# Kernel optimization log

Hardware: AMD Instinct MI355X
Metric: run time of the kernel (lower is better)

The kernel has to match this reference:

```python
import jax, jax.numpy as jnp
import numpy as np
from jax import lax

B, E, H, L, P, IMG, NCLS = 8, 768, 12, 12, 16, 224, 1000
D = E // H
MLP = 4 * E
SCALE = D ** -0.5
NPATCH = (IMG // P) ** 2  # 196
N = NPATCH + 1             # 197 with cls token
INIT_VAL = 0.1


def _ln(x, g, b, eps=1e-5):
    mu = jnp.mean(x, -1, keepdims=True)
    var = jnp.mean((x - mu) ** 2, -1, keepdims=True)
    return (x - mu) / jnp.sqrt(var + eps) * g + b


def _wasserstein(q, cov_q, k, cov_k):
    # 2-Wasserstein distance matrix between diagonal Gaussians (STOSA style)
    mean_term = (-2.0 * jnp.einsum('bhnd,bhmd->bhnm', q, k)
                 + jnp.sum(q * q, -1)[..., :, None]
                 + jnp.sum(k * k, -1)[..., None, :])
    sq_q = jnp.sqrt(jnp.clip(cov_q, 1e-24))
    sq_k = jnp.sqrt(jnp.clip(cov_k, 1e-24))
    cov_term = (-2.0 * jnp.einsum('bhnd,bhmd->bhnm', sq_q, sq_k)
                + jnp.sum(cov_q, -1)[..., :, None]
                + jnp.sum(cov_k, -1)[..., None, :])
    return mean_term + cov_term


def _patch_embed(x, w, b):
    # x: [B,3,IMG,IMG], w: [E,3,P,P] -> [B, NPATCH, E]
    y = lax.conv_general_dilated(x, w, (P, P), 'VALID',
                                 dimension_numbers=('NCHW', 'OIHW', 'NCHW'))
    y = y + b[None, :, None, None]
    return y.reshape(x.shape[0], E, -1).transpose(0, 2, 1)


def _mlp(x, w1, b1, w2, b2):
    return jax.nn.gelu(x @ w1.T + b1, approximate=False) @ w2.T + b2


def setup_inputs() -> dict:
    key = jax.random.key(0)
    ks = jax.random.split(key, 32)
    s = 0.02
    inp = {
        'x': jax.random.normal(ks[0], (B, 3, IMG, IMG), jnp.float32),
        'rel_pos_bias': jax.random.normal(ks[1], (H, N, N), jnp.float32),
        'patch_w': jax.random.normal(ks[2], (E, 3, P, P), jnp.float32) * s,
        'patch_b': jnp.zeros((E,), jnp.float32),
        'cov_patch_w': jax.random.normal(ks[3], (E, 3, P, P), jnp.float32) * s,
        'cov_patch_b': jnp.zeros((E,), jnp.float32),
        'cls_tok': jax.random.normal(ks[4], (1, 1, E), jnp.float32) * s,
        'cov_cls_tok': jax.random.normal(ks[5], (1, 1, E), jnp.float32) * s,
        'norm1_g': jnp.ones((L, E), jnp.float32),
        'norm1_b': jnp.zeros((L, E), jnp.float32),
        'qkv_w': jax.random.normal(ks[6], (L, 3 * E, E), jnp.float32) * s,
        'q_bias': jnp.zeros((L, E), jnp.float32),
        'v_bias': jnp.zeros((L, E), jnp.float32),
        'cov_q_bias': jnp.zeros((L, E), jnp.float32),
        'cov_v_bias': jnp.zeros((L, E), jnp.float32),
        'proj_w': jax.random.normal(ks[7], (L, E, E), jnp.float32) * s,
        'proj_b': jnp.zeros((L, E), jnp.float32),
        'cov_proj_w': jax.random.normal(ks[8], (L, E, E), jnp.float32) * s,
        'cov_proj_b': jnp.zeros((L, E), jnp.float32),
        'gamma1': jnp.full((L, E), INIT_VAL, jnp.float32),
        'gamma2': jnp.full((L, E), INIT_VAL, jnp.float32),
        'norm2_g': jnp.ones((L, E), jnp.float32),
        'norm2_b': jnp.zeros((L, E), jnp.float32),
        'fc1_w': jax.random.normal(ks[9], (L, MLP, E), jnp.float32) * s,
        'fc1_b': jnp.zeros((L, MLP), jnp.float32),
        'fc2_w': jax.random.normal(ks[10], (L, E, MLP), jnp.float32) * s,
        'fc2_b': jnp.zeros((L, E), jnp.float32),
        'fc_norm_g': jnp.ones((E,), jnp.float32),
        'fc_norm_b': jnp.zeros((E,), jnp.float32),
        'head_w': jax.random.normal(ks[11], (NCLS, E), jnp.float32) * s,
        'head_b': jnp.zeros((NCLS,), jnp.float32),
    }
    # fix_init_weight rescaling: proj / cov_proj / fc2 divided by sqrt(2*layer_id)
    resc = 1.0 / jnp.sqrt(2.0 * jnp.arange(1, L + 1, dtype=jnp.float32))
    inp['proj_w'] = inp['proj_w'] * resc[:, None, None]
    inp['cov_proj_w'] = inp['cov_proj_w'] * resc[:, None, None]
    inp['fc2_w'] = inp['fc2_w'] * resc[:, None, None]
    return inp


def reference(x, rel_pos_bias, patch_w, patch_b, cov_patch_w, cov_patch_b,
              cls_tok, cov_cls_tok, norm1_g, norm1_b, qkv_w, q_bias, v_bias,
              cov_q_bias, cov_v_bias, proj_w, proj_b, cov_proj_w, cov_proj_b,
              gamma1, gamma2, norm2_g, norm2_b, fc1_w, fc1_b, fc2_w, fc2_b,
              fc_norm_g, fc_norm_b, head_w, head_b):
    b = x.shape[0]
    xm = _patch_embed(x, patch_w, patch_b)
    xc = _patch_embed(x, cov_patch_w, cov_patch_b)
    xm = jnp.concatenate([jnp.broadcast_to(cls_tok, (b, 1, E)), xm], 1)
    xc = jnp.concatenate([jnp.broadcast_to(cov_cls_tok, (b, 1, E)), xc], 1)
    n = xm.shape[1]

    for i in range(L):
        xm_n = _ln(xm, norm1_g[i], norm1_b[i])
        xc_n = _ln(xc, norm1_g[i], norm1_b[i])  # shared norm1, as in source
        qkvb = jnp.concatenate([q_bias[i], jnp.zeros_like(v_bias[i]), v_bias[i]])
        cov_qkvb = jnp.concatenate([cov_q_bias[i], jnp.zeros_like(cov_v_bias[i]), cov_v_bias[i]])
        qkv = (xm_n @ qkv_w[i].T + qkvb).reshape(b, n, 3, H, D).transpose(2, 0, 3, 1, 4)
        q, k, v = qkv[0], qkv[1], qkv[2]
        # NOTE: source (bug-faithfully) uses qkv.weight for the cov path too
        cqkv = jax.nn.elu(xc_n @ qkv_w[i].T + cov_qkvb) + 1.0
        cqkv = cqkv.reshape(b, n, 3, H, D).transpose(2, 0, 3, 1, 4)
        cq, ck, cv = cqkv[0], cqkv[1], cqkv[2]
        q = q * SCALE
        attn = jax.nn.sigmoid(-_wasserstein(q, cq, k, ck) + 1e-24)
        attn = jax.nn.softmax(attn + rel_pos_bias, axis=-1)  # [B,H,N,N]
        mean_ctx = jnp.einsum('bhnm,bhmd->bhnd', attn, v).transpose(0, 2, 1, 3).reshape(b, n, E)
        cov_ctx = jnp.einsum('bhnm,bhmd->bhnd', attn * attn, cv).transpose(0, 2, 1, 3).reshape(b, n, E)
        mh = mean_ctx @ proj_w[i].T + proj_b[i]
        ch = cov_ctx @ cov_proj_w[i].T + cov_proj_b[i]
        xm = xm + gamma1[i] * mh
        xm = xm + gamma2[i] * _mlp(_ln(xm, norm2_g[i], norm2_b[i]), fc1_w[i], fc1_b[i], fc2_w[i], fc2_b[i])
        xc = xc + gamma1[i] * ch
        xc = xc + gamma2[i] * _mlp(_ln(xc, norm2_g[i], norm2_b[i]), fc1_w[i], fc1_b[i], fc2_w[i], fc2_b[i])

    t = jnp.mean(xm[:, 1:], axis=1)          # mean pooling over patch tokens
    t = _ln(t, fc_norm_g, fc_norm_b)
    return t @ head_w.T + head_b              # [B, num_classes]
```

## Files before the change

### kernel.cpp

```cpp
#include <hip/hip_runtime.h>
#include <hip/hip_bf16.h>
#include <math.h>

#define BB 8
#define EE 768
#define HH 12
#define LL 12
#define DD 64
#define MLPD 3072
#define NN 197
#define NPATCH 196
#define NCLS 1000
#define NROWS (BB*NN)
#define PROWS (BB*NPATCH)
#define MPAD 1664
#define HTILES 13
#define NBH (BB*HH)
#define NP224 224
#define NP256 256
#define SCALE 0.125f

#define MODE_F32   0
#define MODE_ELU1F 1
#define MODE_GELUB 2
#define MODE_RESF  3

typedef __attribute__((ext_vector_type(8))) short bf16x8;
typedef __attribute__((ext_vector_type(4))) float f32x4;

__device__ __forceinline__ unsigned short f2b(float f) {
    union { __hip_bfloat16 h; unsigned short u; } x;
    x.h = __float2bfloat16(f);
    return x.u;
}

__device__ __forceinline__ float b2f(unsigned short u) {
    union { unsigned int i; float f; } x;
    x.i = ((unsigned int)u) << 16;
    return x.f;
}

#define GLD(gptr, lptr) __builtin_amdgcn_global_load_lds( \
    (const __attribute__((address_space(1))) unsigned int*)(gptr), \
    (__attribute__((address_space(3))) unsigned int*)(lptr), 16, 0, 0)

__global__ __launch_bounds__(256) void mfma_gemm2(
    const unsigned short* __restrict__ A0, const unsigned short* __restrict__ A1,
    const unsigned short* __restrict__ W0, const unsigned short* __restrict__ W1,
    const float* __restrict__ bias0, const float* __restrict__ bias1,
    int K, int Nc, int mode0, int mode1,
    const float* __restrict__ gamma,
    const float* __restrict__ resid0, const float* __restrict__ resid1,
    float* __restrict__ Cf0, float* __restrict__ Cf1,
    unsigned short* __restrict__ Cb0, unsigned short* __restrict__ Cb1)
{
    __shared__ unsigned short lA[2][128 * 32];
    __shared__ unsigned short lB[2][128 * 32];
    const int tid  = threadIdx.x;
    const int lane = tid & 63;
    const int wave = tid >> 6;
    const int wm = wave >> 1, wn = wave & 1;
    const int half = blockIdx.y >= HTILES;
    const int mout0 = (blockIdx.y - (half ? HTILES : 0)) * 128;
    const int n0 = blockIdx.x * 128;
    const unsigned short* A = half ? A1 : A0;
    const unsigned short* W = half ? W1 : W0;
    const float* bias = half ? bias1 : bias0;
    const float* resid = half ? resid1 : resid0;
    float* Cf = half ? Cf1 : Cf0;
    unsigned short* Cb = half ? Cb1 : Cb0;
    const int mode = half ? mode1 : mode0;

    const int srow  = lane >> 2;
    const int skoff = (lane & 3) * 8;
    const int fr = lane & 15;
    const int fk = (lane >> 4) * 8;

    auto stage = [&](int bufi, int k0) {
#pragma unroll
        for (int i = 0; i < 2; i++) {
            int chunk = wave * 2 + i;
            int row = chunk * 16 + srow;
            GLD(A + (size_t)(mout0 + row) * K + k0 + skoff, &lA[bufi][chunk * 512]);
            GLD(W + (size_t)(n0 + row) * K + k0 + skoff, &lB[bufi][chunk * 512]);
        }
    };

    f32x4 acc[4][4];
#pragma unroll
    for (int i = 0; i < 4; i++)
#pragma unroll
        for (int j = 0; j < 4; j++) acc[i][j] = (f32x4){0.f, 0.f, 0.f, 0.f};

    const int NT = K >> 5;
    stage(0, 0);
    __syncthreads();
    int cur = 0;
    for (int t = 0; t < NT; t++) {
        if (t + 1 < NT) stage(cur ^ 1, (t + 1) * 32);
        bf16x8 a[4], b[4];
#pragma unroll
        for (int q = 0; q < 4; q++) {
            a[q] = *(const bf16x8*)(&lA[cur][(wm * 64 + q * 16 + fr) * 32 + fk]);
            b[q] = *(const bf16x8*)(&lB[cur][(wn * 64 + q * 16 + fr) * 32 + fk]);
        }
#pragma unroll
        for (int i = 0; i < 4; i++)
#pragma unroll
            for (int j = 0; j < 4; j++)
                acc[i][j] = __builtin_amdgcn_mfma_f32_16x16x32_bf16(a[i], b[j], acc[i][j], 0, 0, 0);
        __syncthreads();
        cur ^= 1;
    }

    const int crow0 = mout0 + wm * 64;
    const int ccol0 = n0 + wn * 64;
    const int lr = (lane >> 4) * 4;
    const int lc = lane & 15;
#pragma unroll
    for (int i = 0; i < 4; i++) {
#pragma unroll
        for (int j = 0; j < 4; j++) {
            int col = ccol0 + j * 16 + lc;
            float bv = bias ? bias[col] : 0.f;
#pragma unroll
            for (int r = 0; r < 4; r++) {
                int row = crow0 + i * 16 + lr + r;
                float v = acc[i][j][r] + bv;
                size_t o = (size_t)row * Nc + col;
                if (mode == MODE_ELU1F) {
                    Cf[o] = (v > 0.f) ? (v + 1.f) : expf(v);
                } else if (mode == MODE_GELUB) {
                    v = 0.5f * v * (1.f + erff(v * 0.70710678118654752f));
                    Cb[o] = f2b(v);
                } else if (mode == MODE_RESF) {
                    Cf[o] = resid[o] + gamma[col] * v;
                } else {
                    Cf[o] = v;
                }
            }
        }
    }
}

__global__ __launch_bounds__(256) void mfma_gemm2_sk(
    const unsigned short* __restrict__ A0, const unsigned short* __restrict__ A1,
    const unsigned short* __restrict__ W0, const unsigned short* __restrict__ W1,
    int K, int Kc, int Nc, int S,
    float* __restrict__ P)
{
    __shared__ unsigned short lA[2][128 * 32];
    __shared__ unsigned short lB[2][128 * 32];
    const int tid  = threadIdx.x;
    const int lane = tid & 63;
    const int wave = tid >> 6;
    const int wm = wave >> 1, wn = wave & 1;
    const int half = blockIdx.y >= HTILES;
    const int mout0 = (blockIdx.y - (half ? HTILES : 0)) * 128;
    const int n0 = blockIdx.x * 128;
    const int z = blockIdx.z;
    const int kb = z * Kc;
    const unsigned short* A = half ? A1 : A0;
    const unsigned short* W = half ? W1 : W0;

    const int srow  = lane >> 2;
    const int skoff = (lane & 3) * 8;
    const int fr = lane & 15;
    const int fk = (lane >> 4) * 8;

    auto stage = [&](int bufi, int k0) {
#pragma unroll
        for (int i = 0; i < 2; i++) {
            int chunk = wave * 2 + i;
            int row = chunk * 16 + srow;
            GLD(A + (size_t)(mout0 + row) * K + k0 + skoff, &lA[bufi][chunk * 512]);
            GLD(W + (size_t)(n0 + row) * K + k0 + skoff, &lB[bufi][chunk * 512]);
        }
    };

    f32x4 acc[4][4];
#pragma unroll
    for (int i = 0; i < 4; i++)
#pragma unroll
        for (int j = 0; j < 4; j++) acc[i][j] = (f32x4){0.f, 0.f, 0.f, 0.f};

    const int NT = Kc >> 5;
    stage(0, kb);
    __syncthreads();
    int cur = 0;
    for (int t = 0; t < NT; t++) {
        if (t + 1 < NT) stage(cur ^ 1, kb + (t + 1) * 32);
        bf16x8 a[4], b[4];
#pragma unroll
        for (int q = 0; q < 4; q++) {
            a[q] = *(const bf16x8*)(&lA[cur][(wm * 64 + q * 16 + fr) * 32 + fk]);
            b[q] = *(const bf16x8*)(&lB[cur][(wn * 64 + q * 16 + fr) * 32 + fk]);
        }
#pragma unroll
        for (int i = 0; i < 4; i++)
#pragma unroll
            for (int j = 0; j < 4; j++)
                acc[i][j] = __builtin_amdgcn_mfma_f32_16x16x32_bf16(a[i], b[j], acc[i][j], 0, 0, 0);
        __syncthreads();
        cur ^= 1;
    }

    float* Pout = P + (size_t)(half * S + z) * MPAD * Nc;
    const int crow0 = mout0 + wm * 64;
    const int ccol0 = n0 + wn * 64;
    const int lr = (lane >> 4) * 4;
    const int lc = lane & 15;
#pragma unroll
    for (int i = 0; i < 4; i++) {
#pragma unroll
        for (int j = 0; j < 4; j++) {
            int col = ccol0 + j * 16 + lc;
#pragma unroll
            for (int r = 0; r < 4; r++) {
                int row = crow0 + i * 16 + lr + r;
                Pout[(size_t)row * Nc + col] = acc[i][j][r];
            }
        }
    }
}

__global__ __launch_bounds__(256) void sk_reduce_kernel(
    const float* __restrict__ P, int S, int Nc,
    const float* __restrict__ bias0, const float* __restrict__ bias1,
    float* __restrict__ C0, float* __restrict__ C1)
{
    const size_t per = (size_t)MPAD * Nc;
    size_t gi = ((size_t)blockIdx.x * 256 + threadIdx.x) * 4;
    if (gi >= per) return;
    const int half = blockIdx.y;
    const float* p = P + (size_t)half * S * per + gi;
    float4 s = *(const float4*)p;
    for (int z = 1; z < S; z++) {
        float4 q = *(const float4*)(p + (size_t)z * per);
        s.x += q.x; s.y += q.y; s.z += q.z; s.w += q.w;
    }
    const int col = (int)(gi % (size_t)Nc);
    const float* bias = half ? bias1 : bias0;
    float4 bv = *(const float4*)(bias + col);
    s.x += bv.x; s.y += bv.y; s.z += bv.z; s.w += bv.w;
    float* C = half ? C1 : C0;
    *(float4*)(C + gi) = s;
}

__global__ __launch_bounds__(256) void sk_reduce_ln(
    const float* __restrict__ P, int S,
    const float* __restrict__ bias0, const float* __restrict__ bias1,
    const float* __restrict__ gamma,
    const float* __restrict__ resid0, const float* __restrict__ resid1,
    float* __restrict__ C0, float* __restrict__ C1,
    const float* __restrict__ lnG, const float* __restrict__ lnB,
    unsigned short* __restrict__ Y)
{
    const int row = blockIdx.x;
    const int half = blockIdx.y;
    const int tid = threadIdx.x;
    const size_t per = (size_t)MPAD * EE;
    const float* p = P + (size_t)half * S * per + (size_t)row * EE;
    const float* bias = half ? bias1 : bias0;
    const float* resid = half ? resid1 : resid0;
    float* C = half ? C1 : C0;
    float v[3];
#pragma unroll
    for (int i = 0; i < 3; i++) {
        int e = tid + i * 256;
        float s = p[e];
        for (int z = 1; z < S; z++) s += p[(size_t)z * per + e];
        v[i] = resid[(size_t)row * EE + e] + gamma[e] * (s + bias[e]);
        C[(size_t)row * EE + e] = v[i];
    }
    if (!Y) return;
    __shared__ float red[256];
    red[tid] = v[0] + v[1] + v[2];
    __syncthreads();
    for (int s2 = 128; s2 > 0; s2 >>= 1) { if (tid < s2) red[tid] += red[tid + s2]; __syncthreads(); }
    float mu = red[0] * (1.f / 768.f);
    __syncthreads();
    float d0 = v[0] - mu, d1 = v[1] - mu, d2 = v[2] - mu;
    red[tid] = d0 * d0 + d1 * d1 + d2 * d2;
    __syncthreads();
    for (int s2 = 128; s2 > 0; s2 >>= 1) { if (tid < s2) red[tid] += red[tid + s2]; __syncthreads(); }
    float rstd = rsqrtf(red[0] * (1.f / 768.f) + 1e-5f);
    unsigned short* yr = Y + ((size_t)half * MPAD + row) * EE;
    yr[tid]       = f2b(d0 * rstd * lnG[tid]       + lnB[tid]);
    yr[tid + 256] = f2b(d1 * rstd * lnG[tid + 256] + lnB[tid + 256]);
    yr[tid + 512] = f2b(d2 * rstd * lnG[tid + 512] + lnB[tid + 512]);
}

__global__ __launch_bounds__(256) void pre_kernel(
    const float* __restrict__ qkv, const float* __restrict__ cqkv,
    unsigned short* __restrict__ Aq, unsigned short* __restrict__ Bk,
    float* __restrict__ rsum, float* __restrict__ csum,
    unsigned short* __restrict__ vT, unsigned short* __restrict__ cvT)
{
    const int t = blockIdx.x;
    const int bh = blockIdx.y;
    const int b = bh / HH, h = bh % HH;
    const int n0 = t * 64;
    const int lane = threadIdx.x & 63;
    const int w = threadIdx.x >> 6;
    __shared__ unsigned short vs[64][66];
    __shared__ unsigned short cvs[64][66];

    for (int p = 0; p < 16; p++) {
        int nl = p * 4 + w;
        int n = n0 + nl;
        int d = lane;
        size_t arow = ((size_t)bh * NP256 + n) * 128;
        if (n < NN) {
            size_t basei = (size_t)(b * NN + n) * 3 * EE + h * DD + d;
            float q  = qkv[basei];
            float k  = qkv[basei + EE];
            float v  = qkv[basei + 2 * EE];
            float cq = cqkv[basei];
            float ck = cqkv[basei + EE];
            float cv = cqkv[basei + 2 * EE];
            float qs = q * SCALE;
            float sqq = sqrtf(fmaxf(cq, 1e-24f));
            float sqk = sqrtf(fmaxf(ck, 1e-24f));
            Aq[arow + d]      = f2b(qs);
            Aq[arow + 64 + d] = f2b(sqq);
            Bk[arow + d]      = f2b(k);
            Bk[arow + 64 + d] = f2b(sqk);
            vs[nl][d]  = f2b(v);
            cvs[nl][d] = f2b(cv);
            float r = qs * qs + cq;
            float c = k * k + ck;
            for (int off2 = 32; off2 > 0; off2 >>= 1) {
                r += __shfl_down(r, off2);
                c += __shfl_down(c, off2);
            }
            if (d == 0) { rsum[bh * NP256 + n] = r; csum[bh * NP256 + n] = c; }
        } else {
            ((unsigned int*)(Aq + arow))[d] = 0u;
            ((unsigned int*)(Bk + arow))[d] = 0u;
            vs[nl][d] = 0; cvs[nl][d] = 0;
            if (d == 0) { rsum[bh * NP256 + n] = 0.f; csum[bh * NP256 + n] = 0.f; }
        }
    }
    __syncthreads();
    for (int p = 0; p < 16; p++) {
        int dr = p * 4 + w;
        int n = n0 + lane;
        if (n < NP224) {
            vT [((size_t)bh * 64 + dr) * NP224 + n] = vs[lane][dr];
            cvT[((size_t)bh * 64 + dr) * NP224 + n] = cvs[lane][dr];
        }
    }
}

#define PADW 232
__global__ __launch_bounds__(256) void attn_fused(
    const unsigned short* __restrict__ Aq, const unsigned short* __restrict__ Bk,
    const float* __restrict__ rsum, const float* __restrict__ csum,
    const float* __restrict__ rpb,
    const unsigned short* __restrict__ vT, const unsigned short* __restrict__ cvT,
    unsigned short* __restrict__ ctxm, unsigned short* __restrict__ ctxc)
{
    __shared__ unsigned short lA[64 * 32];
    __shared__ unsigned short lB[256 * 32];
    __shared__ unsigned short lB2[128 * 32];
    __shared__ unsigned short pL[64 * PADW];
    const int tid = threadIdx.x, lane = tid & 63, w = tid >> 6;
    const int bh = blockIdx.y;
    const int b = bh / HH, h = bh % HH;
    const int q0 = blockIdx.x * 64;
    const int srow = lane >> 2, skoff = (lane & 3) * 8;
    const int fr = lane & 15, fk = (lane >> 4) * 8;
    const int lr4 = (lane >> 4) * 4;
    const unsigned short* A = Aq + (size_t)bh * NP256 * 128;
    const unsigned short* B = Bk + (size_t)bh * NP256 * 128;

    f32x4 accS[16];
#pragma unroll
    for (int j = 0; j < 16; j++) accS[j] = (f32x4){0.f, 0.f, 0.f, 0.f};

    for (int k0 = 0; k0 < 128; k0 += 32) {
        GLD(A + (size_t)(q0 + w * 16 + srow) * 128 + k0 + skoff, lA + w * 512);
#pragma unroll
        for (int i = 0; i < 4; i++) {
            int chunk = w * 4 + i;
            GLD(B + (size_t)(chunk * 16 + srow) * 128 + k0 + skoff, lB + chunk * 512);
        }
        __syncthreads();
        bf16x8 a = *(const bf16x8*)(lA + (w * 16 + fr) * 32 + fk);
#pragma unroll
        for (int j = 0; j < 16; j++) {
            bf16x8 bb = *(const bf16x8*)(lB + (j * 16 + fr) * 32 + fk);
            accS[j] = __builtin_amdgcn_mfma_f32_16x16x32_bf16(a, bb, accS[j], 0, 0, 0);
        }
        __syncthreads();
    }

    float rs[4];
#pragma unroll
    for (int r = 0; r < 4; r++) rs[r] = rsum[bh * NP256 + q0 + w * 16 + lr4 + r];
    float cs[16];
#pragma unroll
    for (int j = 0; j < 16; j++) cs[j] = csum[bh * NP256 + j * 16 + fr];

#pragma unroll
    for (int r = 0; r < 4; r++) {
        int rowg = q0 + w * 16 + lr4 + r;
        float v[16];
#pragma unroll
        for (int j = 0; j < 16; j++) {
            int col = j * 16 + fr;
            float z = 2.f * accS[j][r] - rs[r] - cs[j] + 1e-24f;
            float s = 1.f / (1.f + expf(-z));
            float rp = (col < NN && rowg < NN) ? rpb[((size_t)h * NN + rowg) * NN + col] : 0.f;
            v[j] = (col < NN) ? (s + rp) : -1e30f;
        }
        float mx = -1e30f;
#pragma unroll
        for (int j = 0; j < 16; j++) mx = fmaxf(mx, v[j]);
        mx = fmaxf(mx, __shfl_xor(mx, 1));
        mx = fmaxf(mx, __shfl_xor(mx, 2));
        mx = fmaxf(mx, __shfl_xor(mx, 4));
        mx = fmaxf(mx, __shfl_xor(mx, 8));
        float sum = 0.f;
#pragma unroll
        for (int j = 0; j < 16; j++) { v[j] = expf(v[j] - mx); sum += v[j]; }
        sum += __shfl_xor(sum, 1);
        sum += __shfl_xor(sum, 2);
        sum += __shfl_xor(sum, 4);
        sum += __shfl_xor(sum, 8);
        float inv = 1.f / sum;
        int rowl = w * 16 + lr4 + r;
#pragma unroll
        for (int j = 0; j < 14; j++)
            pL[rowl * PADW + j * 16 + fr] = f2b(v[j] * inv);
    }

    f32x4 acc2[2][4];
#pragma unroll
    for (int p = 0; p < 2; p++)
#pragma unroll
        for (int j = 0; j < 4; j++) acc2[p][j] = (f32x4){0.f, 0.f, 0.f, 0.f};

    for (int k0 = 0; k0 < NP224; k0 += 32) {
#pragma unroll
        for (int i = 0; i < 2; i++) {
            int chunk = w * 2 + i;
            const unsigned short* src = (chunk < 4)
                ? (vT  + ((size_t)bh * 64 + chunk * 16 + srow) * NP224)
                : (cvT + ((size_t)bh * 64 + (chunk - 4) * 16 + srow) * NP224);
            GLD(src + k0 + skoff, lB2 + chunk * 512);
        }
        __syncthreads();
        bf16x8 ap = *(const bf16x8*)(pL + (w * 16 + fr) * PADW + k0 + fk);
        bf16x8 ap2;
#pragma unroll
        for (int e = 0; e < 8; e++) {
            float pv = b2f((unsigned short)ap[e]);
            ap2[e] = (short)f2b(pv * pv);
        }
#pragma unroll
        for (int j = 0; j < 4; j++) {
            bf16x8 bv = *(const bf16x8*)(lB2 + (j * 16 + fr) * 32 + fk);
            bf16x8 bc = *(const bf16x8*)(lB2 + ((64 + j * 16) + fr) * 32 + fk);
            acc2[0][j] = __builtin_amdgcn_mfma_f32_16x16x32_bf16(ap,  bv, acc2[0][j], 0, 0, 0);
            acc2[1][j] = __builtin_amdgcn_mfma_f32_16x16x32_bf16(ap2, bc, acc2[1][j], 0, 0, 0);
        }
        __syncthreads();
    }

#pragma unroll
    for (int j = 0; j < 4; j++) {
        int d = j * 16 + fr;
#pragma unroll
        for (int r = 0; r < 4; r++) {
            int n = q0 + w * 16 + lr4 + r;
            if (n >= NN) continue;
            size_t o = ((size_t)(b * NN + n)) * EE + h * DD + d;
            ctxm[o] = f2b(acc2[0][j][r]);
            ctxc[o] = f2b(acc2[1][j][r]);
        }
    }
}

__global__ __launch_bounds__(256) void head_kernel(
    const float* __restrict__ pooled, const float* __restrict__ W,
    const float* __restrict__ bias, float* __restrict__ out)
{
    const int wv = threadIdx.x >> 6, lane = threadIdx.x & 63;
    const int c = blockIdx.x * 4 + wv;
    const int b = blockIdx.y;
    if (c >= NCLS) return;
    const float* wr = W + (size_t)c * EE;
    const float* pr = pooled + (size_t)b * EE;
    float s = 0.f;
#pragma unroll
    for (int i = 0; i < 12; i++) s += pr[lane + i * 64] * wr[lane + i * 64];
    for (int off = 32; off > 0; off >>= 1) s += __shfl_down(s, off);
    if (lane == 0) out[(size_t)b * NCLS + c] = s + bias[c];
}

__global__ __launch_bounds__(256) void cvt_kernel(
    const float* __restrict__ src, unsigned short* __restrict__ dst, int n)
{
    int i = (blockIdx.x * 256 + threadIdx.x) * 4;
    if (i >= n) return;
    float4 f = *(const float4*)(src + i);
    ushort4 u;
    u.x = f2b(f.x); u.y = f2b(f.y); u.z = f2b(f.z); u.w = f2b(f.w);
    *(ushort4*)(dst + i) = u;
}

#define W_QKV   0
#define W_PROJ  1769472
#define W_CPROJ 2359296
#define W_FC1   2949120
#define W_FC2   5308416
#define W_TOTAL 7667712

__global__ __launch_bounds__(256) void cvt_all_kernel(
    const float* __restrict__ qkvw, const float* __restrict__ pw,
    const float* __restrict__ cpw, const float* __restrict__ f1,
    const float* __restrict__ f2, unsigned short* __restrict__ dst)
{
    size_t i = ((size_t)blockIdx.x * 256 + threadIdx.x) * 4;
    if (i >= (size_t)LL * W_TOTAL) return;
    int l = (int)(i / W_TOTAL);
    int r = (int)(i % W_TOTAL);
    const float* s;
    if (r < W_PROJ)        s = qkvw + (size_t)l * (3 * EE * EE) + r;
    else if (r < W_CPROJ)  s = pw   + (size_t)l * (EE * EE)     + (r - W_PROJ);
    else if (r < W_FC1)    s = cpw  + (size_t)l * (EE * EE)     + (r - W_CPROJ);
    else if (r < W_FC2)    s = f1   + (size_t)l * (MLPD * EE)   + (r - W_FC1);
    else                   s = f2   + (size_t)l * (MLPD * EE)   + (r - W_FC2);
    float4 f = *(const float4*)s;
    ushort4 u;
    u.x = f2b(f.x); u.y = f2b(f.y); u.z = f2b(f.z); u.w = f2b(f.w);
    *(ushort4*)(dst + i) = u;
}

__global__ __launch_bounds__(256) void qkvbias_all_kernel(
    const float* __restrict__ qb, const float* __restrict__ vb,
    const float* __restrict__ cqb, const float* __restrict__ cvb,
    float* __restrict__ bqc)
{
    int l = blockIdx.y;
    int j = blockIdx.x * 256 + threadIdx.x;
    if (j >= 3 * EE) return;
    float m, c;
    if (j < EE)        { m = qb[l * EE + j];          c = cqb[l * EE + j]; }
    else if (j < 2*EE) { m = 0.f;                      c = 0.f; }
    else               { m = vb[l * EE + j - 2 * EE];  c = cvb[l * EE + j - 2 * EE]; }
    bqc[(size_t)l * 4608 + j]        = m;
    bqc[(size_t)l * 4608 + 2304 + j] = c;
}

__global__ __launch_bounds__(256) void im2col_kernel(
    const float* __restrict__ x, unsigned short* __restrict__ col)
{
    int idx = blockIdx.x * 256 + threadIdx.x;
    if (idx >= PROWS * EE) return;
    int c = idx % EE;
    int r = idx / EE;
    int b = r / NPATCH;
    int p = r % NPATCH;
    int ph = p / 14, pw = p % 14;
    int ch = c >> 8;
    int rem = c & 255;
    int i = rem >> 4, j = rem & 15;
    col[idx] = f2b(x[(((size_t)b * 3 + ch) * 224 + (ph * 16 + i)) * 224 + (pw * 16 + j)]);
}

__global__ __launch_bounds__(256) void assemble_kernel(
    const float* __restrict__ tm, const float* __restrict__ tc,
    const float* __restrict__ cls, const float* __restrict__ ccls,
    float* __restrict__ xm, float* __restrict__ xc)
{
    int idx = blockIdx.x * 256 + threadIdx.x;
    if (idx >= NROWS * EE) return;
    int e = idx % EE;
    int r = idx / EE;
    int b = r / NN, n = r % NN;
    if (n == 0) {
        xm[idx] = cls[e];
        xc[idx] = ccls[e];
    } else {
        size_t s = ((size_t)(b * NPATCH + n - 1)) * EE + e;
        xm[idx] = tm[s];
        xc[idx] = tc[s];
    }
}

__global__ __launch_bounds__(256) void ln2_kernel(
    const float* __restrict__ xm, const float* __restrict__ xc,
    unsigned short* __restrict__ y, const float* __restrict__ g,
    const float* __restrict__ bb)
{
    int row = blockIdx.x;
    int tid = threadIdx.x;
    const float* src;
    size_t orow;
    if (row < NROWS) { src = xm + (size_t)row * EE; orow = row; }
    else { src = xc + (size_t)(row - NROWS) * EE; orow = (size_t)(row - NROWS) + MPAD; }
    __shared__ float red[256];
    float v0 = src[tid], v1 = src[tid + 256], v2 = src[tid + 512];
    red[tid] = v0 + v1 + v2;
    __syncthreads();
    for (int s = 128; s > 0; s >>= 1) { if (tid < s) red[tid] += red[tid + s]; __syncthreads(); }
    float mu = red[0] * (1.f / 768.f);
    __syncthreads();
    float d0 = v0 - mu, d1 = v1 - mu, d2 = v2 - mu;
    red[tid] = d0 * d0 + d1 * d1 + d2 * d2;
    __syncthreads();
    for (int s = 128; s > 0; s >>= 1) { if (tid < s) red[tid] += red[tid + s]; __syncthreads(); }
    float rstd = rsqrtf(red[0] * (1.f / 768.f) + 1e-5f);
    unsigned short* yr = y + orow * EE;
    yr[tid]       = f2b(d0 * rstd * g[tid]       + bb[tid]);
    yr[tid + 256] = f2b(d1 * rstd * g[tid + 256] + bb[tid + 256]);
    yr[tid + 512] = f2b(d2 * rstd * g[tid + 512] + bb[tid + 512]);
}

__global__ __launch_bounds__(256) void pool_ln_kernel(
    const float* __restrict__ xm, float* __restrict__ out,
    const float* __restrict__ g, const float* __restrict__ bb)
{
    int b = blockIdx.x;
    int tid = threadIdx.x;
    __shared__ float red[256];
    float p[3];
#pragma unroll
    for (int i = 0; i < 3; i++) {
        int e = tid + i * 256;
        float s = 0.f;
        for (int n = 1; n < NN; n++) s += xm[((size_t)(b * NN + n)) * EE + e];
        p[i] = s * (1.f / 196.f);
    }
    red[tid] = p[0] + p[1] + p[2];
    __syncthreads();
    for (int s = 128; s > 0; s >>= 1) { if (tid < s) red[tid] += red[tid + s]; __syncthreads(); }
    float mu = red[0] * (1.f / 768.f);
    __syncthreads();
    float d0 = p[0] - mu, d1 = p[1] - mu, d2 = p[2] - mu;
    red[tid] = d0 * d0 + d1 * d1 + d2 * d2;
    __syncthreads();
    for (int s = 128; s > 0; s >>= 1) { if (tid < s) red[tid] += red[tid + s]; __syncthreads(); }
    float rstd = rsqrtf(red[0] * (1.f / 768.f) + 1e-5f);
    out[(size_t)b * EE + tid]       = d0 * rstd * g[tid]       + bb[tid];
    out[(size_t)b * EE + tid + 256] = d1 * rstd * g[tid + 256] + bb[tid + 256];
    out[(size_t)b * EE + tid + 512] = d2 * rstd * g[tid + 512] + bb[tid + 512];
}

extern "C" void kernel_launch(void* const* d_in, const int* in_sizes, int n_in,
                              void* d_out, int out_size, void* d_ws, size_t ws_size,
                              hipStream_t stream)
{
    const float* x        = (const float*)d_in[0];
    const float* rpb      = (const float*)d_in[1];
    const float* patch_w  = (const float*)d_in[2];
    const float* patch_b  = (const float*)d_in[3];
    const float* cpatch_w = (const float*)d_in[4];
    const float* cpatch_b = (const float*)d_in[5];
    const float* cls_tok  = (const float*)d_in[6];
    const float* ccls_tok = (const float*)d_in[7];
    const float* norm1_g  = (const float*)d_in[8];
    const float* norm1_b  = (const float*)d_in[9];
    const float* qkv_w    = (const float*)d_in[10];
    const float* q_bias   = (const float*)d_in[11];
    const float* v_bias   = (const float*)d_in[12];
    const float* cq_bias  = (const float*)d_in[13];
    const float* cv_bias  = (const float*)d_in[14];
    const float* proj_w   = (const float*)d_in[15];
    const float* proj_b   = (const float*)d_in[16];
    const float* cproj_w  = (const float*)d_in[17];
    const float* cproj_b  = (const float*)d_in[18];
    const float* gamma1   = (const float*)d_in[19];
    const float* gamma2   = (const float*)d_in[20];
    const float* norm2_g  = (const float*)d_in[21];
    const float* norm2_b  = (const float*)d_in[22];
    const float* fc1_w    = (const float*)d_in[23];
    const float* fc1_b    = (const float*)d_in[24];
    const float* fc2_w    = (const float*)d_in[25];
    const float* fc2_b    = (const float*)d_in[26];
    const float* fcn_g    = (const float*)d_in[27];
    const float* fcn_b    = (const float*)d_in[28];
    const float* head_w   = (const float*)d_in[29];
    const float* head_b   = (const float*)d_in[30];
    float* out = (float*)d_out;

    char* base = (char*)d_ws;
    size_t off = 0;
    auto alloc = [&](size_t bytes) {
        void* p = base + off;
        off = (off + bytes + 255) & ~(size_t)255;
        return p;
    };
    unsigned short* wbuf  = (unsigned short*)alloc((size_t)LL * W_TOTAL * 2);
    unsigned short* pw_m  = (unsigned short*)alloc((size_t)589824 * 2);
    unsigned short* pw_c  = (unsigned short*)alloc((size_t)589824 * 2);
    float* xm   = (float*)alloc((size_t)MPAD * EE * 4);
    float* xc   = (float*)alloc((size_t)MPAD * EE * 4);
    unsigned short* xn2 = (unsigned short*)alloc((size_t)2 * MPAD * EE * 2);
    float* qkv  = (float*)alloc((size_t)MPAD * 3 * EE * 4);
    float* cqkv = (float*)alloc((size_t)MPAD * 3 * EE * 4);
    unsigned short* hbuf = (unsigned short*)alloc((size_t)2 * MPAD * MLPD * 2);
    unsigned short* Aq  = (unsigned short*)alloc((size_t)NBH * NP256 * 128 * 2);
    unsigned short* Bk  = (unsigned short*)alloc((size_t)NBH * NP256 * 128 * 2);
    unsigned short* vT  = (unsigned short*)alloc((size_t)NBH * 64 * NP224 * 2);
    unsigned short* cvT = (unsigned short*)alloc((size_t)NBH * 64 * NP224 * 2);
    float* rsum = (float*)alloc((size_t)NBH * NP256 * 4);
    float* csum = (float*)alloc((size_t)NBH * NP256 * 4);
    unsigned short* ctx2 = (unsigned short*)alloc((size_t)2 * MPAD * EE * 2);
    unsigned short* colb = (unsigned short*)alloc((size_t)MPAD * EE * 2);
    float* bqc    = (float*)alloc((size_t)LL * 2 * 2304 * 4);
    float* pooled = (float*)alloc((size_t)BB * EE * 4);
    float* pbuf = (float*)alloc((size_t)2 * 4 * MPAD * EE * 4);
    float* tm = qkv;
    float* tc = cqkv;
    unsigned short* ctxm = ctx2;
    unsigned short* ctxc = ctx2 + (size_t)MPAD * EE;

    dim3 t256(256);
    dim3 gridRedE(MPAD * EE / 1024, 2);
    dim3 gridRedLN(MPAD, 2);

    {
        size_t tot4 = (size_t)LL * W_TOTAL / 4;
        cvt_all_kernel<<<dim3((unsigned)((tot4 + 255) / 256)), t256, 0, stream>>>(
            qkv_w, proj_w, cproj_w, fc1_w, fc2_w, wbuf);
        qkvbias_all_kernel<<<dim3(9, LL), t256, 0, stream>>>(
            q_bias, v_bias, cq_bias, cv_bias, bqc);
    }

    cvt_kernel<<<dim3(589824 / 4 / 256), t256, 0, stream>>>(patch_w, pw_m, 589824);
    cvt_kernel<<<dim3(589824 / 4 / 256), t256, 0, stream>>>(cpatch_w, pw_c, 589824);
    im2col_kernel<<<dim3((PROWS * EE + 255) / 256), t256, 0, stream>>>(x, colb);
    mfma_gemm2_sk<<<dim3(EE / 128, 2 * HTILES, 3), t256, 0, stream>>>(
        colb, colb, pw_m, pw_c, EE, 256, EE, 3, pbuf);
    sk_reduce_kernel<<<gridRedE, t256, 0, stream>>>(
        pbuf, 3, EE, patch_b, cpatch_b, tm, tc);
    assemble_kernel<<<dim3((NROWS * EE + 255) / 256), t256, 0, stream>>>(
        tm, tc, cls_tok, ccls_tok, xm, xc);
    ln2_kernel<<<dim3(2 * NROWS), t256, 0, stream>>>(xm, xc, xn2, norm1_g, norm1_b);

    dim3 gridQKV(3 * EE / 128, 2 * HTILES);
    dim3 gridMLP(MLPD / 128, 2 * HTILES);
    dim3 gridPre(4, NBH);
    dim3 gridAttn(4, NBH);
    const unsigned short* xn2c = xn2 + (size_t)MPAD * EE;
    const unsigned short* hbufc = hbuf + (size_t)MPAD * MLPD;

    for (int l = 0; l < LL; l++) {
        const unsigned short* wl = wbuf + (size_t)l * W_TOTAL;
        const float* biasq = bqc + (size_t)l * 4608;
        const float* biasc = biasq + 2304;

        mfma_gemm2<<<gridQKV, t256, 0, stream>>>(
            xn2, xn2c, wl + W_QKV, wl + W_QKV, biasq, biasc, EE, 3 * EE,
            MODE_F32, MODE_ELU1F, nullptr, nullptr, nullptr, qkv, cqkv, nullptr, nullptr);

        pre_kernel<<<gridPre, t256, 0, stream>>>(qkv, cqkv, Aq, Bk, rsum, csum, vT, cvT);
        attn_fused<<<gridAttn, t256, 0, stream>>>(Aq, Bk, rsum, csum, rpb, vT, cvT, ctxm, ctxc);

        mfma_gemm2_sk<<<dim3(EE / 128, 2 * HTILES, 3), t256, 0, stream>>>(
            ctxm, ctxc, wl + W_PROJ, wl + W_CPROJ, EE, 256, EE, 3, pbuf);
        sk_reduce_ln<<<gridRedLN, t256, 0, stream>>>(
            pbuf, 3, proj_b + l * EE, cproj_b + l * EE,
            gamma1 + l * EE, xm, xc, xm, xc,
            norm2_g + l * EE, norm2_b + l * EE, xn2);

        mfma_gemm2<<<gridMLP, t256, 0, stream>>>(
            xn2, xn2c, wl + W_FC1, wl + W_FC1, fc1_b + l * MLPD, fc1_b + l * MLPD,
            EE, MLPD, MODE_GELUB, MODE_GELUB, nullptr, nullptr, nullptr,
            nullptr, nullptr, hbuf, hbuf + (size_t)MPAD * MLPD);
        mfma_gemm2_sk<<<dim3(EE / 128, 2 * HTILES, 4), t256, 0, stream>>>(
            hbuf, hbufc, wl + W_FC2, wl + W_FC2, MLPD, 768, EE, 4, pbuf);
        if (l + 1 < LL) {
            sk_reduce_ln<<<gridRedLN, t256, 0, stream>>>(
                pbuf, 4, fc2_b + l * EE, fc2_b + l * EE,
                gamma2 + l * EE, xm, xc, xm, xc,
                norm1_g + (l + 1) * EE, norm1_b + (l + 1) * EE, xn2);
        } else {
            sk_reduce_ln<<<gridRedLN, t256, 0, stream>>>(
                pbuf, 4, fc2_b + l * EE, fc2_b + l * EE,
                gamma2 + l * EE, xm, xc, xm, xc,
                nullptr, nullptr, nullptr);
        }
    }

    pool_ln_kernel<<<dim3(BB), t256, 0, stream>>>(xm, pooled, fcn_g, fcn_b);
    head_kernel<<<dim3((NCLS + 3) / 4, BB), t256, 0, stream>>>(pooled, head_w, head_b, out);
}
```

Measured before the change: 2.654 ms.

## Merge weight conversions into one kernel, deepen FC2 split-K, parallelize pooling

```diff
diff --git a/kernel.cpp b/kernel.cpp
--- a/kernel.cpp
+++ b/kernel.cpp
@@ -500,43 +500,51 @@
     if (lane == 0) out[(size_t)b * NCLS + c] = s + bias[c];
 }
 
-__global__ __launch_bounds__(256) void cvt_kernel(
-    const float* __restrict__ src, unsigned short* __restrict__ dst, int n)
-{
-    int i = (blockIdx.x * 256 + threadIdx.x) * 4;
-    if (i >= n) return;
-    float4 f = *(const float4*)(src + i);
-    ushort4 u;
-    u.x = f2b(f.x); u.y = f2b(f.y); u.z = f2b(f.z); u.w = f2b(f.w);
-    *(ushort4*)(dst + i) = u;
-}
-
 #define W_QKV   0
 #define W_PROJ  1769472
 #define W_CPROJ 2359296
 #define W_FC1   2949120
 #define W_FC2   5308416
 #define W_TOTAL 7667712
+#define PW_ELEMS 589824
 
 __global__ __launch_bounds__(256) void cvt_all_kernel(
     const float* __restrict__ qkvw, const float* __restrict__ pw,
     const float* __restrict__ cpw, const float* __restrict__ f1,
-    const float* __restrict__ f2, unsigned short* __restrict__ dst)
-{
-    size_t i = ((size_t)blockIdx.x * 256 + threadIdx.x) * 4;
-    if (i >= (size_t)LL * W_TOTAL) return;
-    int l = (int)(i / W_TOTAL);
-    int r = (int)(i % W_TOTAL);
-    const float* s;
-    if (r < W_PROJ)        s = qkvw + (size_t)l * (3 * EE * EE) + r;
-    else if (r < W_CPROJ)  s = pw   + (size_t)l * (EE * EE)     + (r - W_PROJ);
-    else if (r < W_FC1)    s = cpw  + (size_t)l * (EE * EE)     + (r - W_CPROJ);
-    else if (r < W_FC2)    s = f1   + (size_t)l * (MLPD * EE)   + (r - W_FC1);
-    else                   s = f2   + (size_t)l * (MLPD * EE)   + (r - W_FC2);
-    float4 f = *(const float4*)s;
-    ushort4 u;
-    u.x = f2b(f.x); u.y = f2b(f.y); u.z = f2b(f.z); u.w = f2b(f.w);
-    *(ushort4*)(dst + i) = u;
+    const float* __restrict__ f2,
+    const float* __restrict__ patchw, const float* __restrict__ cpatchw,
+    unsigned short* __restrict__ dst,
+    unsigned short* __restrict__ dpw, unsigned short* __restrict__ dcpw)
+{
+    const size_t NW  = (size_t)LL * W_TOTAL;
+    const size_t TOT = NW + 2 * (size_t)PW_ELEMS;
+    const size_t stride = (size_t)gridDim.x * 256 * 8;
+    for (size_t i = ((size_t)blockIdx.x * 256 + threadIdx.x) * 8; i < TOT; i += stride) {
+        const float* s;
+        unsigned short* d;
+        if (i < NW) {
+            int l = (int)(i / W_TOTAL);
+            int r = (int)(i % W_TOTAL);
+            if (r < W_PROJ)        s = qkvw + (size_t)l * (3 * EE * EE) + r;
+            else if (r < W_CPROJ)  s = pw   + (size_t)l * (EE * EE)     + (r - W_PROJ);
+            else if (r < W_FC1)    s = cpw  + (size_t)l * (EE * EE)     + (r - W_CPROJ);
+            else if (r < W_FC2)    s = f1   + (size_t)l * (MLPD * EE)   + (r - W_FC1);
+            else                   s = f2   + (size_t)l * (MLPD * EE)   + (r - W_FC2);
+            d = dst + i;
+        } else if (i < NW + PW_ELEMS) {
+            size_t r = i - NW;
+            s = patchw + r; d = dpw + r;
+        } else {
+            size_t r = i - NW - PW_ELEMS;
+            s = cpatchw + r; d = dcpw + r;
+        }
+        float4 fa = *(const float4*)s;
+        float4 fb = *(const float4*)(s + 4);
+        union { ushort4 u4[2]; unsigned int w[4]; } o;
+        o.u4[0].x = f2b(fa.x); o.u4[0].y = f2b(fa.y); o.u4[0].z = f2b(fa.z); o.u4[0].w = f2b(fa.w);
+        o.u4[1].x = f2b(fb.x); o.u4[1].y = f2b(fb.y); o.u4[1].z = f2b(fb.z); o.u4[1].w = f2b(fb.w);
+        *(uint4*)d = *(const uint4*)o.w;
+    }
 }
 
 __global__ __launch_bounds__(256) void qkvbias_all_kernel(
@@ -626,14 +634,25 @@
 {
     int b = blockIdx.x;
     int tid = threadIdx.x;
+    int w = tid >> 6, lane = tid & 63;
+    __shared__ float part[4][768];
+    float acc[12];
+#pragma unroll
+    for (int i = 0; i < 12; i++) acc[i] = 0.f;
+    for (int n = w; n < NPATCH; n += 4) {
+        const float* row = xm + ((size_t)(b * NN + 1 + n)) * EE;
+#pragma unroll
+        for (int i = 0; i < 12; i++) acc[i] += row[lane + i * 64];
+    }
+#pragma unroll
+    for (int i = 0; i < 12; i++) part[w][lane + i * 64] = acc[i];
+    __syncthreads();
     __shared__ float red[256];
     float p[3];
 #pragma unroll
     for (int i = 0; i < 3; i++) {
         int e = tid + i * 256;
-        float s = 0.f;
-        for (int n = 1; n < NN; n++) s += xm[((size_t)(b * NN + n)) * EE + e];
-        p[i] = s * (1.f / 196.f);
+        p[i] = (part[0][e] + part[1][e] + part[2][e] + part[3][e]) * (1.f / 196.f);
     }
     red[tid] = p[0] + p[1] + p[2];
     __syncthreads();
@@ -695,8 +714,8 @@
         return p;
     };
     unsigned short* wbuf  = (unsigned short*)alloc((size_t)LL * W_TOTAL * 2);
-    unsigned short* pw_m  = (unsigned short*)alloc((size_t)589824 * 2);
-    unsigned short* pw_c  = (unsigned short*)alloc((size_t)589824 * 2);
+    unsigned short* pw_m  = (unsigned short*)alloc((size_t)PW_ELEMS * 2);
+    unsigned short* pw_c  = (unsigned short*)alloc((size_t)PW_ELEMS * 2);
     float* xm   = (float*)alloc((size_t)MPAD * EE * 4);
     float* xc   = (float*)alloc((size_t)MPAD * EE * 4);
     unsigned short* xn2 = (unsigned short*)alloc((size_t)2 * MPAD * EE * 2);
@@ -713,7 +732,7 @@
     unsigned short* colb = (unsigned short*)alloc((size_t)MPAD * EE * 2);
     float* bqc    = (float*)alloc((size_t)LL * 2 * 2304 * 4);
     float* pooled = (float*)alloc((size_t)BB * EE * 4);
-    float* pbuf = (float*)alloc((size_t)2 * 4 * MPAD * EE * 4);
+    float* pbuf = (float*)alloc((size_t)2 * 6 * MPAD * EE * 4);
     float* tm = qkv;
     float* tc = cqkv;
     unsigned short* ctxm = ctx2;
@@ -723,16 +742,11 @@
     dim3 gridRedE(MPAD * EE / 1024, 2);
     dim3 gridRedLN(MPAD, 2);
 
-    {
-        size_t tot4 = (size_t)LL * W_TOTAL / 4;
-        cvt_all_kernel<<<dim3((unsigned)((tot4 + 255) / 256)), t256, 0, stream>>>(
-            qkv_w, proj_w, cproj_w, fc1_w, fc2_w, wbuf);
-        qkvbias_all_kernel<<<dim3(9, LL), t256, 0, stream>>>(
-            q_bias, v_bias, cq_bias, cv_bias, bqc);
-    }
-
-    cvt_kernel<<<dim3(589824 / 4 / 256), t256, 0, stream>>>(patch_w, pw_m, 589824);
-    cvt_kernel<<<dim3(589824 / 4 / 256), t256, 0, stream>>>(cpatch_w, pw_c, 589824);
+    cvt_all_kernel<<<dim3(4096), t256, 0, stream>>>(
+        qkv_w, proj_w, cproj_w, fc1_w, fc2_w, patch_w, cpatch_w, wbuf, pw_m, pw_c);
+    qkvbias_all_kernel<<<dim3(9, LL), t256, 0, stream>>>(
+        q_bias, v_bias, cq_bias, cv_bias, bqc);
+
     im2col_kernel<<<dim3((PROWS * EE + 255) / 256), t256, 0, stream>>>(x, colb);
     mfma_gemm2_sk<<<dim3(EE / 128, 2 * HTILES, 3), t256, 0, stream>>>(
         colb, colb, pw_m, pw_c, EE, 256, EE, 3, pbuf);
@@ -772,16 +786,16 @@
             xn2, xn2c, wl + W_FC1, wl + W_FC1, fc1_b + l * MLPD, fc1_b + l * MLPD,
             EE, MLPD, MODE_GELUB, MODE_GELUB, nullptr, nullptr, nullptr,
             nullptr, nullptr, hbuf, hbuf + (size_t)MPAD * MLPD);
-        mfma_gemm2_sk<<<dim3(EE / 128, 2 * HTILES, 4), t256, 0, stream>>>(
-            hbuf, hbufc, wl + W_FC2, wl + W_FC2, MLPD, 768, EE, 4, pbuf);
+        mfma_gemm2_sk<<<dim3(EE / 128, 2 * HTILES, 6), t256, 0, stream>>>(
+            hbuf, hbufc, wl + W_FC2, wl + W_FC2, MLPD, 512, EE, 6, pbuf);
         if (l + 1 < LL) {
             sk_reduce_ln<<<gridRedLN, t256, 0, stream>>>(
-                pbuf, 4, fc2_b + l * EE, fc2_b + l * EE,
+                pbuf, 6, fc2_b + l * EE, fc2_b + l * EE,
                 gamma2 + l * EE, xm, xc, xm, xc,
                 norm1_g + (l + 1) * EE, norm1_b + (l + 1) * EE, xn2);
         } else {
             sk_reduce_ln<<<gridRedLN, t256, 0, stream>>>(
-                pbuf, 4, fc2_b + l * EE, fc2_b + l * EE,
+                pbuf, 6, fc2_b + l * EE, fc2_b + l * EE,
                 gamma2 + l * EE, xm, xc, xm, xc,
                 nullptr, nullptr, nullptr);
         }
```

After: 2.741 ms. 1.03x slower.
